# Performance work log

Measured on AMD Instinct MI355X. Metric: run time of the kernel, lower is better.

## Reference

```python
import jax, jax.numpy as jnp
import numpy as np

DIM = 4096
NH = 32       # query heads
NKV = 8       # kv heads
HD = DIM // NH  # 128
B = 1
S = 2048
ROPE_BASE = 10000.0


def rope_tables(seq_len, head_dim, base=ROPE_BASE):
    inv_freq = 1.0 / base ** (jnp.arange(0, head_dim, 2, dtype=jnp.float32) / head_dim)
    t = jnp.arange(seq_len, dtype=jnp.float32)
    freqs = jnp.einsum('i,j->ij', t, inv_freq)          # [S, HD/2]
    emb = jnp.concatenate([freqs, freqs], axis=-1)      # [S, HD]
    return jnp.cos(emb), jnp.sin(emb)


def apply_rope(x, cos, sin):
    # x: [B, H, S, HD]; matches torch apply_rotary_emb (chunk halves)
    x1, x2 = jnp.split(x, 2, axis=-1)
    d = x1.shape[-1]
    c = cos[None, None, :, :d]
    s = sin[None, None, :, :d]
    return jnp.concatenate([x1 * c - x2 * s, x2 * c + x1 * s], axis=-1)


def setup_inputs() -> dict:
    key = jax.random.key(0)
    k0, k1, k2, k3, k4 = jax.random.split(key, 5)
    sc = 0.02  # typical init scale for stable softmax
    return {
        'x': jax.random.normal(k0, (B, S, DIM), jnp.float32),
        'wq': jax.random.normal(k1, (DIM, NH * HD), jnp.float32) * sc,
        'wk': jax.random.normal(k2, (DIM, NKV * HD), jnp.float32) * sc,
        'wv': jax.random.normal(k3, (DIM, NKV * HD), jnp.float32) * sc,
        'wo': jax.random.normal(k4, (NH * HD, DIM), jnp.float32) * sc,
        'mask': jnp.ones((1,), jnp.bool_),  # presence triggers is_causal=True in torch SDPA path
    }


def reference(x, wq, wk, wv, wo, mask):
    Bsz, Sl, _ = x.shape
    n_rep = NH // NKV
    q = (x @ wq).reshape(Bsz, Sl, NH, HD).transpose(0, 2, 1, 3)    # [B,NH,S,HD]
    k = (x @ wk).reshape(Bsz, Sl, NKV, HD).transpose(0, 2, 1, 3)   # [B,NKV,S,HD]
    v = (x @ wv).reshape(Bsz, Sl, NKV, HD).transpose(0, 2, 1, 3)
    cos, sin = rope_tables(Sl, HD)
    q = apply_rope(q, cos, sin)
    k = apply_rope(k, cos, sin)
    # GQA without repeat_interleave: group query heads per kv head
    qg = q.reshape(Bsz, NKV, n_rep, Sl, HD)
    scale = HD ** -0.5
    scores = jnp.einsum('bgrqd,bgkd->bgrqk', qg, k) * scale        # [B,NKV,n_rep,S,S]
    causal = jnp.tril(jnp.ones((Sl, Sl), dtype=bool))
    scores = jnp.where(causal[None, None, None], scores, jnp.finfo(scores.dtype).min)
    attn = jax.nn.softmax(scores, axis=-1)
    out = jnp.einsum('bgrqk,bgkd->bgrqd', attn, v)                 # [B,NKV,n_rep,S,HD]
    out = out.reshape(Bsz, NH, Sl, HD).transpose(0, 2, 1, 3).reshape(Bsz, Sl, NH * HD)
    return out @ wo
```

## Files before the change

### kernel.cpp

```cpp
#include <hip/hip_runtime.h>
#include <hip/hip_bf16.h>
#include <cstdint>
#include <cmath>

#define DIM 4096
#define NH 32
#define NKV 8
#define HD 128
#define S_LEN 2048
#define KVD (NKV * HD)
#define QS 6144
#define SCALE 0.08838834764831845f

typedef __attribute__((ext_vector_type(4))) float f32x4;
typedef __attribute__((ext_vector_type(8))) short short8;

__device__ __forceinline__ short f2bf(float f) {
  union { float f; uint32_t u; } v; v.f = f;
  uint32_t u = v.u;
  u += 0x7fffu + ((u >> 16) & 1u);
  return (short)(u >> 16);
}
__device__ __forceinline__ float bf2f(short b) {
  union { uint32_t u; float f; } v; v.u = ((uint32_t)(uint16_t)b) << 16;
  return v.f;
}

__device__ __forceinline__ void async16(const void* g, void* l) {
  __builtin_amdgcn_global_load_lds(
      (__attribute__((address_space(1))) void*)(g),
      (__attribute__((address_space(3))) void*)(l), 16, 0, 0);
}


__global__ void rope_tables_k(float* __restrict__ ct, float* __restrict__ st) {
  const int i = blockIdx.x * blockDim.x + threadIdx.x;
  if (i >= S_LEN * 64) return;
  const int s = i >> 6, d = i & 63;
  const float inv = powf(10000.0f, -(float)(2 * d) / 128.0f);
  const float fr = (float)s * inv;
  ct[i] = cosf(fr);
  st[i] = sinf(fr);
}

__global__ void cast_f32_bf16_k(const float* __restrict__ in, short* __restrict__ out, int n4) {
  const int i = blockIdx.x * blockDim.x + threadIdx.x;
  if (i >= n4) return;
  const float4 v = ((const float4*)in)[i];
  short4 o;
  o.x = f2bf(v.x); o.y = f2bf(v.y); o.z = f2bf(v.z); o.w = f2bf(v.w);
  ((short4*)out)[i] = o;
}

__global__ __launch_bounds__(256) void prep_w_k(
    const float* __restrict__ wq, const float* __restrict__ wk,
    const float* __restrict__ wv, const float* __restrict__ wo,
    short* __restrict__ wqkvT, short* __restrict__ woT) {
  __shared__ float tile[64][65];
  int b = blockIdx.x;
  const float* src; short* dst; int N, bx, by;
  if (b < 4096)      { src = wq; dst = wqkvT;                        N = 4096; bx = b & 63; by = b >> 6; }
  else if (b < 5120) { b -= 4096; src = wk; dst = wqkvT + (size_t)4096 * DIM; N = 1024; bx = b & 15; by = b >> 4; }
  else if (b < 6144) { b -= 5120; src = wv; dst = wqkvT + (size_t)5120 * DIM; N = 1024; bx = b & 15; by = b >> 4; }
  else               { b -= 6144; src = wo; dst = woT;               N = 4096; bx = b & 63; by = b >> 6; }
  const int r0 = by * 64, c0 = bx * 64;
  const int tx = threadIdx.x, ty = threadIdx.y;
#pragma unroll
  for (int j = 0; j < 16; ++j)
    tile[ty + j * 4][tx] = src[(size_t)(r0 + ty + j * 4) * N + c0 + tx];
  __syncthreads();
#pragma unroll
  for (int j = 0; j < 16; ++j)
    dst[(size_t)(c0 + ty + j * 4) * DIM + r0 + tx] = f2bf(tile[tx][ty + j * 4]);
}

__global__ void transpose_bf16_k(const short* __restrict__ in, short* __restrict__ out,
                                 int R, int C, int ldi) {
  __shared__ short tile[32][33];
  const int tx = threadIdx.x, ty = threadIdx.y;
  const int c0 = blockIdx.x * 32, r0 = blockIdx.y * 32;
#pragma unroll
  for (int j = 0; j < 4; ++j)
    tile[ty + j * 8][tx] = in[(size_t)(r0 + ty + j * 8) * ldi + c0 + tx];
  __syncthreads();
#pragma unroll
  for (int j = 0; j < 4; ++j)
    out[(size_t)(c0 + ty + j * 8) * R + r0 + tx] = tile[tx][ty + j * 8];
}

__global__ void rope_apply_k(short* __restrict__ xq, int ld, const float* __restrict__ ct,
                             const float* __restrict__ st, int nheads) {
  const int i = blockIdx.x * blockDim.x + threadIdx.x;
  const int total = S_LEN * nheads * 64;
  if (i >= total) return;
  const int d = i & 63;
  const int t = i >> 6;
  const int hh = t % nheads;
  const int s = t / nheads;
  short* p = xq + (size_t)s * ld + hh * HD + d;
  const float x1 = bf2f(p[0]);
  const float x2 = bf2f(p[64]);
  const float c = ct[(s << 6) + d];
  const float sn = st[(s << 6) + d];
  p[0]  = f2bf(x1 * c - x2 * sn);
  p[64] = f2bf(x2 * c + x1 * sn);
}

#define SYNC2(VM, LG)                                            \
  asm volatile("s_waitcnt vmcnt(" #VM ")" ::: "memory");         \
  __builtin_amdgcn_s_barrier();                                  \
  asm volatile("s_waitcnt lgkmcnt(" #LG ")" ::: "memory");       \
  __builtin_amdgcn_sched_barrier(0);                             \
  __builtin_amdgcn_s_setprio(1)

#define PH_END()                                                 \
  __builtin_amdgcn_s_setprio(0);                                 \
  __builtin_amdgcn_sched_barrier(0);                             \
  __builtin_amdgcn_s_barrier()


__global__ __launch_bounds__(512, 2) void gemm192_k(
    const short* __restrict__ A, const short* __restrict__ BT,
    short* __restrict__ C, int M, int N, int K) {
  __shared__ __attribute__((aligned(16))) short ldsA[2][256 * 64];
  __shared__ __attribute__((aligned(16))) short ldsB[2][192 * 64];
  const int tid = threadIdx.x;
  const int l = tid & 63, w = tid >> 6;
  const int wrM = w >> 1, wcN = w & 1;
  const int lrow = l & 15, lg = l >> 4;
  const int cofs[2] = {(lg ^ (lrow & 7)) << 3, ((4 + lg) ^ (lrow & 7)) << 3};
  (void)M;

  int bid = blockIdx.x;
  const int cpx = gridDim.x >> 3;
  bid = (bid & 7) * cpx + (bid >> 3);
  const int ntn = N / 192;
  const int m0 = (bid / ntn) << 8;
  const int n0 = (bid % ntn) * 192;

  auto stage = [&](int tau) {
    const int k0 = tau << 6;
    short* bd = &ldsB[tau & 1][0];
    short* ad = &ldsA[tau & 1][0];
#pragma unroll
    for (int it = 0; it < 3; ++it) {
      const int e = it * 512 + tid;
      const int row = e >> 3;
      const int js = (e & 7) ^ (row & 7);
      async16(BT + (size_t)(n0 + row) * K + k0 + js * 8, bd + e * 8);
    }
#pragma unroll
    for (int it = 0; it < 4; ++it) {
      const int e = it * 512 + tid;
      const int row = e >> 3;
      const int js = (e & 7) ^ (row & 7);
      async16(A + (size_t)(m0 + row) * K + k0 + js * 8, ad + e * 8);
    }
  };
  auto rdA = [&](short8 (&dst)[4][2], int b) {
    const short* p = &ldsA[b][0];
#pragma unroll
    for (int mi = 0; mi < 4; ++mi) {
      const int row = wrM * 64 + mi * 16 + lrow;
#pragma unroll
      for (int kk = 0; kk < 2; ++kk)
        dst[mi][kk] = *(const short8*)(p + row * 64 + cofs[kk]);
    }
  };
  auto rdB = [&](short8 (&dst)[2][2], int b, int pr) {
    const short* p = &ldsB[b][0];
#pragma unroll
    for (int ni = 0; ni < 2; ++ni) {
      const int row = wcN * 96 + pr * 32 + ni * 16 + lrow;
#pragma unroll
      for (int kk = 0; kk < 2; ++kk)
        dst[ni][kk] = *(const short8*)(p + row * 64 + cofs[kk]);
    }
  };

  f32x4 acc[4][6] = {};
  auto third = [&](short8 (&Af)[4][2], int pr, short8 (&Bf)[2][2]) {
#pragma unroll
    for (int kk = 0; kk < 2; ++kk)
#pragma unroll
      for (int mi = 0; mi < 4; ++mi)
#pragma unroll
        for (int ni = 0; ni < 2; ++ni)
          acc[mi][pr * 2 + ni] = __builtin_amdgcn_mfma_f32_16x16x32_bf16(
              Af[mi][kk], Bf[ni][kk], acc[mi][pr * 2 + ni], 0, 0, 0);
  };

  short8 Aa[4][2], Ab[4][2], B0f[2][2], B1f[2][2], B2f[2][2];

  stage(0); stage(1);
  asm volatile("s_waitcnt vmcnt(7)" ::: "memory");
  __builtin_amdgcn_s_barrier();
  rdB(B0f, 0, 0);
  rdA(Aa, 0);

  const int KT = K >> 6;
  for (int u = 0; u < (KT - 2) / 2; ++u) {
    const int e = 2 * u;
    rdB(B1f, 0, 1); rdB(B2f, 0, 2);
    SYNC2(7, 8);  third(Aa, 0, B0f); PH_END();
    SYNC2(0, 0);  stage(e + 2); third(Aa, 1, B1f); PH_END();
    rdB(B0f, 1, 0); rdA(Ab, 1);
    SYNC2(7, 12); third(Aa, 2, B2f); PH_END();
    rdB(B1f, 1, 1); rdB(B2f, 1, 2);
    SYNC2(7, 8);  third(Ab, 0, B0f); PH_END();
    SYNC2(0, 0);  stage(e + 3); third(Ab, 1, B1f); PH_END();
    rdB(B0f, 0, 0); rdA(Aa, 0);
    SYNC2(7, 12); third(Ab, 2, B2f); PH_END();
  }
  rdB(B1f, 0, 1); rdB(B2f, 0, 2);
  SYNC2(7, 8);  third(Aa, 0, B0f); PH_END();
  SYNC2(0, 0);  third(Aa, 1, B1f); PH_END();
  rdB(B0f, 1, 0); rdA(Ab, 1);
  SYNC2(0, 12); third(Aa, 2, B2f); PH_END();
  rdB(B1f, 1, 1); rdB(B2f, 1, 2);
  SYNC2(0, 8);  third(Ab, 0, B0f); PH_END();
  SYNC2(0, 0);  third(Ab, 1, B1f); PH_END();
  SYNC2(0, 0);  third(Ab, 2, B2f); PH_END();

  const int orow0 = m0 + wrM * 64 + lg * 4;
  const int ocol0 = n0 + wcN * 96 + lrow;
#pragma unroll
  for (int mi = 0; mi < 4; ++mi)
#pragma unroll
    for (int n = 0; n < 6; ++n)
#pragma unroll
      for (int r = 0; r < 4; ++r)
        C[(size_t)(orow0 + mi * 16 + r) * N + (ocol0 + n * 16)] = f2bf(acc[mi][n][r]);
}


__global__ __launch_bounds__(512, 2) void gemm_wo2_k(
    const short* __restrict__ A, const short* __restrict__ BT,
    float* __restrict__ C, int M, int N, int K) {
  __shared__ __attribute__((aligned(16))) short ldsA[2][128 * 64];
  __shared__ __attribute__((aligned(16))) short ldsB[2][256 * 64];
  const int tid = threadIdx.x;
  const int l = tid & 63, w = tid >> 6;
  const int wrM = w >> 2, wcN = w & 3;
  const int lrow = l & 15, lg = l >> 4;
  const int cofs[2] = {(lg ^ (lrow & 7)) << 3, ((4 + lg) ^ (lrow & 7)) << 3};
  (void)M;

  int bid = blockIdx.x;
  const int cpx = gridDim.x >> 3;
  bid = (bid & 7) * cpx + (bid >> 3);
  const int ntn = N >> 8;
  const int m0 = (bid / ntn) << 7;
  const int n0 = (bid % ntn) << 8;

  auto stage = [&](int tau) {
    const int k0 = tau << 6;
    short* ad = &ldsA[tau & 1][0];
    short* bd = &ldsB[tau & 1][0];
#pragma unroll
    for (int it = 0; it < 2; ++it) {
      const int e = it * 512 + tid;
      const int row = e >> 3;
      const int js = (e & 7) ^ (row & 7);
      async16(A + (size_t)(m0 + row) * K + k0 + js * 8, ad + e * 8);
    }
#pragma unroll
    for (int it = 0; it < 4; ++it) {
      const int e = it * 512 + tid;
      const int row = e >> 3;
      const int js = (e & 7) ^ (row & 7);
      async16(BT + (size_t)(n0 + row) * K + k0 + js * 8, bd + e * 8);
    }
  };
  auto rdA = [&](short8 (&dst)[4][2], int b) {
    const short* p = &ldsA[b][0];
#pragma unroll
    for (int mi = 0; mi < 4; ++mi) {
      const int row = wrM * 64 + mi * 16 + lrow;
#pragma unroll
      for (int kk = 0; kk < 2; ++kk)
        dst[mi][kk] = *(const short8*)(p + row * 64 + cofs[kk]);
    }
  };
  auto rdB = [&](short8 (&dst)[2][2], int b, int h) {
    const short* p = &ldsB[b][0];
#pragma unroll
    for (int ni = 0; ni < 2; ++ni) {
      const int row = wcN * 64 + h * 32 + ni * 16 + lrow;
#pragma unroll
      for (int kk = 0; kk < 2; ++kk)
        dst[ni][kk] = *(const short8*)(p + row * 64 + cofs[kk]);
    }
  };

  f32x4 acc[4][4] = {};
  auto half = [&](short8 (&Af)[4][2], int h, short8 (&Bf)[2][2]) {
#pragma unroll
    for (int kk = 0; kk < 2; ++kk)
#pragma unroll
      for (int mi = 0; mi < 4; ++mi)
#pragma unroll
        for (int ni = 0; ni < 2; ++ni)
          acc[mi][h * 2 + ni] = __builtin_amdgcn_mfma_f32_16x16x32_bf16(
              Af[mi][kk], Bf[ni][kk], acc[mi][h * 2 + ni], 0, 0, 0);
  };

  short8 Aa[4][2], Ab[4][2], H0[2][2], H1[2][2];

  stage(0); stage(1);
  asm volatile("s_waitcnt vmcnt(6)" ::: "memory");
  __builtin_amdgcn_s_barrier();
  rdA(Aa, 0); rdB(H0, 0, 0);

  const int KT = K >> 6;
  for (int u = 0; u < (KT - 2) / 2; ++u) {
    const int e = 2 * u;
    rdB(H1, 0, 1);
    SYNC2(6, 4);  half(Aa, 0, H0); PH_END();
    SYNC2(0, 0);  stage(e + 2); rdA(Ab, 1); rdB(H0, 1, 0);
                  half(Aa, 1, H1); PH_END();
    rdB(H1, 1, 1);
    SYNC2(6, 4);  half(Ab, 0, H0); PH_END();
    SYNC2(0, 0);  stage(e + 3); rdA(Aa, 0); rdB(H0, 0, 0);
                  half(Ab, 1, H1); PH_END();
  }
  rdB(H1, 0, 1);
  SYNC2(6, 4);  half(Aa, 0, H0); PH_END();
  SYNC2(0, 0);  rdA(Ab, 1); rdB(H0, 1, 0);
                half(Aa, 1, H1); PH_END();
  rdB(H1, 1, 1);
  SYNC2(0, 4);  half(Ab, 0, H0); PH_END();
  SYNC2(0, 0);  half(Ab, 1, H1); PH_END();

  const int orow0 = m0 + wrM * 64 + lg * 4;
  const int ocol0 = n0 + wcN * 64 + lrow;
#pragma unroll
  for (int mi = 0; mi < 4; ++mi)
#pragma unroll
    for (int n = 0; n < 4; ++n)
#pragma unroll
      for (int r = 0; r < 4; ++r)
        C[(size_t)(orow0 + mi * 16 + r) * N + (ocol0 + n * 16)] = acc[mi][n][r];
}


__global__ __launch_bounds__(256, 3) void attn_k(
    const short* __restrict__ Q, const short* __restrict__ Kc,
    const short* __restrict__ VTg, short* __restrict__ O) {
  __shared__ __attribute__((aligned(16))) short Ks[2][64 * 128];
  __shared__ __attribute__((aligned(16))) short Vt[2][128 * 64];
  __shared__ __attribute__((aligned(16))) short Ps[4][32 * 64];

  const int tid = threadIdx.x;
  const int w = tid >> 6, l = tid & 63;
  const int lrow = l & 15, lg = l >> 4;

  int b = blockIdx.x, h, qt;
  if (b < 256) { h = b >> 3; qt = 15 - (b & 7); }
  else { b -= 256; h = b >> 3; qt = b & 7; }
  const int kvh = h >> 2;
  const int qb0 = qt * 128;
  const int qrow0 = qb0 + w * 32;
  const int nkt = 2 * qt + 2;

  short8 qf[2][4];
#pragma unroll
  for (int nq = 0; nq < 2; ++nq) {
    const short* qp = Q + (size_t)(qrow0 + nq * 16 + lrow) * QS + h * HD;
#pragma unroll
    for (int c = 0; c < 4; ++c) qf[nq][c] = *(const short8*)(qp + c * 32 + lg * 8);
  }

  f32x4 o_acc[2][8] = {};
  float m[2] = {-INFINITY, -INFINITY};
  float lsum[2] = {0.f, 0.f};

  auto stage = [&](int kb, int buf) {
    short* kd = Ks[buf];
    short* vd = Vt[buf];
#pragma unroll
    for (int it = 0; it < 4; ++it) {
      const int e = it * 256 + tid;
      const int row = e >> 4, j = e & 15;
      const int jsrc = (j & 8) | ((j ^ row) & 7);
      async16(Kc + (size_t)(kb + row) * QS + kvh * HD + jsrc * 8, kd + e * 8);
    }
#pragma unroll
    for (int it = 0; it < 4; ++it) {
      const int e = it * 256 + tid;
      const int d = e >> 3, j = e & 7;
      const int jsrc = (j ^ d) & 7;
      async16(VTg + (size_t)(kvh * HD + d) * S_LEN + kb + jsrc * 8, vd + e * 8);
    }
  };

  stage(0, 0);
  int cur = 0;

  for (int kt = 0; kt < nkt; ++kt) {
    __syncthreads();
    if (kt + 1 < nkt) stage((kt + 1) * 64, cur ^ 1);
    const int kb = kt * 64;

    if (kb <= qrow0 + 31) {
      const char* ks = (const char*)Ks[cur];
      const char* vt = (const char*)Vt[cur];
      char* psb = (char*)Ps[w];

      f32x4 stq[4][2] = {};
#pragma unroll
      for (int c = 0; c < 4; ++c) {
#pragma unroll
        for (int mk = 0; mk < 4; ++mk) {
          const short8 kf = *(const short8*)(
              ks + (mk * 16 + lrow) * 256 + (((c * 4 + lg) ^ (lrow & 7)) << 4));
          stq[mk][0] = __builtin_amdgcn_mfma_f32_16x16x32_bf16(kf, qf[0][c], stq[mk][0], 0, 0, 0);
          stq[mk][1] = __builtin_amdgcn_mfma_f32_16x16x32_bf16(kf, qf[1][c], stq[mk][1], 0, 0, 0);
        }
      }

      const bool needmask = (kb + 63 > qrow0);
#pragma unroll
      for (int mk = 0; mk < 4; ++mk)
#pragma unroll
        for (int nq = 0; nq < 2; ++nq)
#pragma unroll
          for (int r = 0; r < 4; ++r) {
            float v = stq[mk][nq][r] * SCALE;
            if (needmask && (kb + mk * 16 + lg * 4 + r > qrow0 + nq * 16 + lrow))
              v = -INFINITY;
            stq[mk][nq][r] = v;
          }

      float vmax[2];
#pragma unroll
      for (int nq = 0; nq < 2; ++nq) {
        float v = stq[0][nq][0];
#pragma unroll
        for (int mk = 0; mk < 4; ++mk)
#pragma unroll
          for (int r = 0; r < 4; ++r) v = fmaxf(v, stq[mk][nq][r]);
        v = fmaxf(v, __shfl_xor(v, 16));
        v = fmaxf(v, __shfl_xor(v, 32));
        vmax[nq] = v;
      }

      const int small = (vmax[0] <= m[0] + 8.0f) && (vmax[1] <= m[1] + 8.0f);
      if (!__all(small)) {
        float al[2];
#pragma unroll
        for (int nq = 0; nq < 2; ++nq) {
          const float mn = fmaxf(m[nq], vmax[nq]);
          al[nq] = __expf(m[nq] - mn);
          m[nq] = mn;
          lsum[nq] *= al[nq];
        }
#pragma unroll
        for (int mmq = 0; mmq < 2; ++mmq)
#pragma unroll
          for (int r = 0; r < 4; ++r) {
            const float a = __shfl(al[mmq], lg * 4 + r);
#pragma unroll
            for (int d = 0; d < 8; ++d) o_acc[mmq][d][r] *= a;
          }
      }

      float rs[2] = {0.f, 0.f};
#pragma unroll
      for (int nq = 0; nq < 2; ++nq) {
#pragma unroll
        for (int mk = 0; mk < 4; ++mk) {
          const float p0 = __expf(stq[mk][nq][0] - m[nq]);
          const float p1 = __expf(stq[mk][nq][1] - m[nq]);
          const float p2 = __expf(stq[mk][nq][2] - m[nq]);
          const float p3 = __expf(stq[mk][nq][3] - m[nq]);
          rs[nq] += (p0 + p1) + (p2 + p3);
          __hip_bfloat16 b0 = __float2bfloat16(p0), b1 = __float2bfloat16(p1);
          __hip_bfloat16 b2 = __float2bfloat16(p2), b3 = __float2bfloat16(p3);
          short4 pk;
          pk.x = *(short*)&b0; pk.y = *(short*)&b1; pk.z = *(short*)&b2; pk.w = *(short*)&b3;
          const int q = nq * 16 + lrow;
          *(short4*)(psb + q * 128 + ((mk * 32 + lg * 8) ^ ((q & 7) << 4))) = pk;
        }
        float r2 = rs[nq];
        r2 += __shfl_xor(r2, 16);
        r2 += __shfl_xor(r2, 32);
        lsum[nq] += r2;
      }

#pragma unroll
      for (int cc = 0; cc < 2; ++cc) {
        const int chunk = ((cc * 4 + lg) ^ (lrow & 7)) << 4;
        const short8 pa0 = *(const short8*)(psb + lrow * 128 + chunk);
        const short8 pa1 = *(const short8*)(psb + (16 + lrow) * 128 + chunk);
#pragma unroll
        for (int d = 0; d < 8; ++d) {
          const short8 vf = *(const short8*)(vt + (d * 16 + lrow) * 128 + chunk);
          o_acc[0][d] = __builtin_amdgcn_mfma_f32_16x16x32_bf16(pa0, vf, o_acc[0][d], 0, 0, 0);
          o_acc[1][d] = __builtin_amdgcn_mfma_f32_16x16x32_bf16(pa1, vf, o_acc[1][d], 0, 0, 0);
        }
      }
    }
    cur ^= 1;
  }

  float linv[2] = {1.0f / lsum[0], 1.0f / lsum[1]};
#pragma unroll
  for (int mmq = 0; mmq < 2; ++mmq)
#pragma unroll
    for (int r = 0; r < 4; ++r) {
      const float li = __shfl(linv[mmq], lg * 4 + r);
      short* op = O + (size_t)(qrow0 + mmq * 16 + lg * 4 + r) * DIM + h * HD;
#pragma unroll
      for (int d = 0; d < 8; ++d)
        op[d * 16 + lrow] = f2bf(o_acc[mmq][d][r] * li);
    }
}


extern "C" void kernel_launch(void* const* d_in, const int* in_sizes, int n_in,
                              void* d_out, int out_size, void* d_ws, size_t ws_size,
                              hipStream_t stream) {
  const float* x  = (const float*)d_in[0];
  const float* wq = (const float*)d_in[1];
  const float* wk = (const float*)d_in[2];
  const float* wv = (const float*)d_in[3];
  const float* wo = (const float*)d_in[4];
  float* out = (float*)d_out;
  (void)in_sizes; (void)n_in; (void)out_size; (void)ws_size;

  char* ws = (char*)d_ws;
  size_t off = 0;
  auto alloc = [&](size_t bytes) -> void* {
    void* p = ws + off;
    off += (bytes + 255) & ~(size_t)255;
    return p;
  };
  short* xb     = (short*)alloc((size_t)S_LEN * DIM * 2);
  short* wqkvT  = (short*)alloc((size_t)QS * DIM * 2);
  short* woT    = (short*)alloc((size_t)DIM * DIM * 2);
  short* qkv    = (short*)alloc((size_t)S_LEN * QS * 2);
  short* vtg    = (short*)alloc((size_t)KVD * S_LEN * 2);
  short* ao     = (short*)alloc((size_t)S_LEN * DIM * 2);
  float* ct     = (float*)alloc((size_t)S_LEN * 64 * 4);
  float* st     = (float*)alloc((size_t)S_LEN * 64 * 4);

  rope_tables_k<<<(S_LEN * 64) / 256, 256, 0, stream>>>(ct, st);
  cast_f32_bf16_k<<<(S_LEN * DIM / 4) / 256, 256, 0, stream>>>(x, xb, S_LEN * DIM / 4);
  prep_w_k<<<dim3(10240), dim3(64, 4), 0, stream>>>(wq, wk, wv, wo, wqkvT, woT);

  gemm192_k<<<dim3((S_LEN / 256) * (QS / 192)), 512, 0, stream>>>(
      xb, wqkvT, qkv, S_LEN, QS, DIM);

  rope_apply_k<<<(S_LEN * 40 * 64) / 256, 256, 0, stream>>>(qkv, QS, ct, st, 40);

  transpose_bf16_k<<<dim3(KVD / 32, S_LEN / 32), dim3(32, 8), 0, stream>>>(
      qkv + 5120, vtg, S_LEN, KVD, QS);

  attn_k<<<dim3(512), 256, 0, stream>>>(qkv, qkv + 4096, vtg, ao);

  gemm_wo2_k<<<dim3((S_LEN / 128) * (DIM / 256)), 512, 0, stream>>>(
      ao, woT, out, S_LEN, DIM, DIM);
}
```

Baseline: 333.1 us.

## Split A/B global staging and restructure QKV GEMM into two-phase schedule

In both bf16 GEMM kernels, the global-to-LDS staging of A and B tiles is split into separate calls. The A load is issued one phase earlier than the B load, so loads are spread across compute phases and waitcnt values change to match. The QKV GEMM also moves from three B sub-tiles of 32 columns to two halves of 48 columns, which means fewer barrier phases per k-step. The risks are a race on LDS buffer reuse if the vmcnt values are wrong, and higher register pressure from the larger B fragments.

After: 318.2 us. -4.5%, faster.

```diff
diff --git a/kernel.cpp b/kernel.cpp
--- a/kernel.cpp
+++ b/kernel.cpp
@@ -138,10 +138,20 @@
   const int m0 = (bid / ntn) << 8;
   const int n0 = (bid % ntn) * 192;
 
-  auto stage = [&](int tau) {
+  auto stageA = [&](int tau) {
+    const int k0 = tau << 6;
+    short* ad = &ldsA[tau & 1][0];
+#pragma unroll
+    for (int it = 0; it < 4; ++it) {
+      const int e = it * 512 + tid;
+      const int row = e >> 3;
+      const int js = (e & 7) ^ (row & 7);
+      async16(A + (size_t)(m0 + row) * K + k0 + js * 8, ad + e * 8);
+    }
+  };
+  auto stageB = [&](int tau) {
     const int k0 = tau << 6;
     short* bd = &ldsB[tau & 1][0];
-    short* ad = &ldsA[tau & 1][0];
 #pragma unroll
     for (int it = 0; it < 3; ++it) {
       const int e = it * 512 + tid;
@@ -149,13 +159,6 @@
       const int js = (e & 7) ^ (row & 7);
       async16(BT + (size_t)(n0 + row) * K + k0 + js * 8, bd + e * 8);
     }
-#pragma unroll
-    for (int it = 0; it < 4; ++it) {
-      const int e = it * 512 + tid;
-      const int row = e >> 3;
-      const int js = (e & 7) ^ (row & 7);
-      async16(A + (size_t)(m0 + row) * K + k0 + js * 8, ad + e * 8);
-    }
   };
   auto rdA = [&](short8 (&dst)[4][2], int b) {
     const short* p = &ldsA[b][0];
@@ -167,11 +170,11 @@
         dst[mi][kk] = *(const short8*)(p + row * 64 + cofs[kk]);
     }
   };
-  auto rdB = [&](short8 (&dst)[2][2], int b, int pr) {
+  auto rdB3 = [&](short8 (&dst)[3][2], int b, int h) {
     const short* p = &ldsB[b][0];
 #pragma unroll
-    for (int ni = 0; ni < 2; ++ni) {
-      const int row = wcN * 96 + pr * 32 + ni * 16 + lrow;
+    for (int ni = 0; ni < 3; ++ni) {
+      const int row = wcN * 96 + h * 48 + ni * 16 + lrow;
 #pragma unroll
       for (int kk = 0; kk < 2; ++kk)
         dst[ni][kk] = *(const short8*)(p + row * 64 + cofs[kk]);
@@ -179,48 +182,43 @@
   };
 
   f32x4 acc[4][6] = {};
-  auto third = [&](short8 (&Af)[4][2], int pr, short8 (&Bf)[2][2]) {
+  auto half24 = [&](short8 (&Af)[4][2], int h, short8 (&Bf)[3][2]) {
 #pragma unroll
     for (int kk = 0; kk < 2; ++kk)
 #pragma unroll
       for (int mi = 0; mi < 4; ++mi)
 #pragma unroll
-        for (int ni = 0; ni < 2; ++ni)
-          acc[mi][pr * 2 + ni] = __builtin_amdgcn_mfma_f32_16x16x32_bf16(
-              Af[mi][kk], Bf[ni][kk], acc[mi][pr * 2 + ni], 0, 0, 0);
-  };
-
-  short8 Aa[4][2], Ab[4][2], B0f[2][2], B1f[2][2], B2f[2][2];
-
-  stage(0); stage(1);
+        for (int ni = 0; ni < 3; ++ni)
+          acc[mi][h * 3 + ni] = __builtin_amdgcn_mfma_f32_16x16x32_bf16(
+              Af[mi][kk], Bf[ni][kk], acc[mi][h * 3 + ni], 0, 0, 0);
+  };
+
+  short8 Aa[4][2], Ab[4][2], BF[3][2], BS[3][2];
+
+  stageA(0); stageB(0); stageA(1); stageB(1);
   asm volatile("s_waitcnt vmcnt(7)" ::: "memory");
   __builtin_amdgcn_s_barrier();
-  rdB(B0f, 0, 0);
-  rdA(Aa, 0);
+  rdA(Aa, 0); rdB3(BF, 0, 0);
 
   const int KT = K >> 6;
   for (int u = 0; u < (KT - 2) / 2; ++u) {
     const int e = 2 * u;
-    rdB(B1f, 0, 1); rdB(B2f, 0, 2);
-    SYNC2(7, 8);  third(Aa, 0, B0f); PH_END();
-    SYNC2(0, 0);  stage(e + 2); third(Aa, 1, B1f); PH_END();
-    rdB(B0f, 1, 0); rdA(Ab, 1);
-    SYNC2(7, 12); third(Aa, 2, B2f); PH_END();
-    rdB(B1f, 1, 1); rdB(B2f, 1, 2);
-    SYNC2(7, 8);  third(Ab, 0, B0f); PH_END();
-    SYNC2(0, 0);  stage(e + 3); third(Ab, 1, B1f); PH_END();
-    rdB(B0f, 0, 0); rdA(Aa, 0);
-    SYNC2(7, 12); third(Ab, 2, B2f); PH_END();
+    rdB3(BS, 0, 1);
+    SYNC2(7, 6);  stageA(e + 2); half24(Aa, 0, BF); PH_END();
+    SYNC2(4, 0);  stageB(e + 2); rdA(Ab, 1); rdB3(BF, 1, 0);
+                  half24(Aa, 1, BS); PH_END();
+    rdB3(BS, 1, 1);
+    SYNC2(7, 6);  stageA(e + 3); half24(Ab, 0, BF); PH_END();
+    SYNC2(4, 0);  stageB(e + 3); rdA(Aa, 0); rdB3(BF, 0, 0);
+                  half24(Ab, 1, BS); PH_END();
   }
-  rdB(B1f, 0, 1); rdB(B2f, 0, 2);
-  SYNC2(7, 8);  third(Aa, 0, B0f); PH_END();
-  SYNC2(0, 0);  third(Aa, 1, B1f); PH_END();
-  rdB(B0f, 1, 0); rdA(Ab, 1);
-  SYNC2(0, 12); third(Aa, 2, B2f); PH_END();
-  rdB(B1f, 1, 1); rdB(B2f, 1, 2);
-  SYNC2(0, 8);  third(Ab, 0, B0f); PH_END();
-  SYNC2(0, 0);  third(Ab, 1, B1f); PH_END();
-  SYNC2(0, 0);  third(Ab, 2, B2f); PH_END();
+  rdB3(BS, 0, 1);
+  SYNC2(7, 6);  half24(Aa, 0, BF); PH_END();
+  SYNC2(0, 0);  rdA(Ab, 1); rdB3(BF, 1, 0);
+                half24(Aa, 1, BS); PH_END();
+  rdB3(BS, 1, 1);
+  SYNC2(0, 6);  half24(Ab, 0, BF); PH_END();
+  SYNC2(0, 0);  half24(Ab, 1, BS); PH_END();
 
   const int orow0 = m0 + wrM * 64 + lg * 4;
   const int ocol0 = n0 + wcN * 96 + lrow;
@@ -253,10 +251,9 @@
   const int m0 = (bid / ntn) << 7;
   const int n0 = (bid % ntn) << 8;
 
-  auto stage = [&](int tau) {
+  auto stageA2 = [&](int tau) {
     const int k0 = tau << 6;
     short* ad = &ldsA[tau & 1][0];
-    short* bd = &ldsB[tau & 1][0];
 #pragma unroll
     for (int it = 0; it < 2; ++it) {
       const int e = it * 512 + tid;
@@ -264,6 +261,10 @@
       const int js = (e & 7) ^ (row & 7);
       async16(A + (size_t)(m0 + row) * K + k0 + js * 8, ad + e * 8);
     }
+  };
+  auto stageB2 = [&](int tau) {
+    const int k0 = tau << 6;
+    short* bd = &ldsB[tau & 1][0];
 #pragma unroll
     for (int it = 0; it < 4; ++it) {
       const int e = it * 512 + tid;
@@ -307,7 +308,7 @@
 
   short8 Aa[4][2], Ab[4][2], H0[2][2], H1[2][2];
 
-  stage(0); stage(1);
+  stageA2(0); stageB2(0); stageA2(1); stageB2(1);
   asm volatile("s_waitcnt vmcnt(6)" ::: "memory");
   __builtin_amdgcn_s_barrier();
   rdA(Aa, 0); rdB(H0, 0, 0);
@@ -316,12 +317,12 @@
   for (int u = 0; u < (KT - 2) / 2; ++u) {
     const int e = 2 * u;
     rdB(H1, 0, 1);
-    SYNC2(6, 4);  half(Aa, 0, H0); PH_END();
-    SYNC2(0, 0);  stage(e + 2); rdA(Ab, 1); rdB(H0, 1, 0);
+    SYNC2(6, 4);  stageA2(e + 2); half(Aa, 0, H0); PH_END();
+    SYNC2(2, 0);  stageB2(e + 2); rdA(Ab, 1); rdB(H0, 1, 0);
                   half(Aa, 1, H1); PH_END();
     rdB(H1, 1, 1);
-    SYNC2(6, 4);  half(Ab, 0, H0); PH_END();
-    SYNC2(0, 0);  stage(e + 3); rdA(Aa, 0); rdB(H0, 0, 0);
+    SYNC2(6, 4);  stageA2(e + 3); half(Ab, 0, H0); PH_END();
+    SYNC2(2, 0);  stageB2(e + 3); rdA(Aa, 0); rdB(H0, 0, 0);
                   half(Ab, 1, H1); PH_END();
   }
   rdB(H1, 0, 1);
```
